# Performance work log

Hardware: AMD Instinct MI355X
Metric: run time of the kernel (lower is better)

Reference implementation:

```python
import jax, jax.numpy as jnp
import numpy as np

EPS = 1e-5
C_M, C, C_Z = 256, 32, 128
N_SEQ, N_RES = 256, 1024


def setup_inputs() -> dict:
    key = jax.random.key(0)
    k1, k2, k3 = jax.random.split(key, 3)
    msa = jax.random.normal(k1, (N_SEQ, N_RES, C_M), dtype=jnp.float32)
    norm_w = jnp.ones((C_M,), dtype=jnp.float32)
    norm_b = jnp.zeros((C_M,), dtype=jnp.float32)
    w_ab = jax.random.normal(k2, (C, C_M), dtype=jnp.float32) * (1.0 / np.sqrt(C_M))
    b_ab = jnp.zeros((C,), dtype=jnp.float32)
    w_out = jax.random.normal(k3, (C_Z, C * C), dtype=jnp.float32) * (1.0 / C)
    b_out = jnp.zeros((C_Z,), dtype=jnp.float32)
    return {"msa": msa, "norm_w": norm_w, "norm_b": norm_b,
            "w_ab": w_ab, "b_ab": b_ab, "w_out": w_out, "b_out": b_out}


def reference(msa, norm_w, norm_b, w_ab, b_ab, w_out, b_out):
    # msa: (s, r, c_m) -> (r, s, c_m)
    x = jnp.transpose(msa, (1, 0, 2))
    s = x.shape[1]
    # LayerNorm over c_m
    mu = jnp.mean(x, axis=-1, keepdims=True)
    var = jnp.mean(jnp.square(x - mu), axis=-1, keepdims=True)
    xn = (x - mu) * jax.lax.rsqrt(var + EPS) * norm_w + norm_b
    # a == b: same linear applied twice to same input in the original
    a = jnp.einsum('rsm,cm->rsc', xn, w_ab) + b_ab          # (r, s, c)
    # mean over s of outer product == batched A^T A / s  -> (r, c, c)
    o = jnp.einsum('rsx,rsy->rxy', a, a) / s
    o = o.reshape(o.shape[0], C * C)                        # (r, c*c)
    pre_pair = jnp.einsum('rk,zk->rz', o, w_out) + b_out    # (r, c_z)
    r = pre_pair.shape[0]
    # unsqueeze(1).expand(r, r, c_z)
    pair = jnp.broadcast_to(pre_pair[:, None, :], (r, r, C_Z))
    return pair
```

## Files before the change

kernel.cpp:

```cpp
#include <hip/hip_runtime.h>

#define NSEQ 256
#define NRES 1024
#define CM   256
#define CC   32
#define CZ   128
#define EPS  1e-5f
#define SROW (NRES * CM)

typedef float f4v __attribute__((ext_vector_type(4)));
typedef __attribute__((ext_vector_type(8))) short short8;
typedef __attribute__((ext_vector_type(4))) float f32x4;
typedef unsigned int u32;

__device__ __forceinline__ float trunc_bf16(float f) {
    return __uint_as_float(__float_as_uint(f) & 0xffff0000u);
}
__device__ __forceinline__ u32 pk_bf16(float a, float b) {
    return (__float_as_uint(b) & 0xffff0000u) | (__float_as_uint(a) >> 16);
}

__global__ void opm_setup(const float* __restrict__ nw,
                          const float* __restrict__ nb,
                          const float* __restrict__ w_ab,
                          const float* __restrict__ b_ab,
                          float* __restrict__ k12,
                          unsigned short* __restrict__ wb_su)
{
    __shared__ float wls[CM * CC];
    const int t = threadIdx.x;
    const float nwm = nw[t];
    #pragma unroll
    for (int c = 0; c < CC; ++c)
        wls[t * CC + c] = nwm * w_ab[c * CM + t];
    __syncthreads();
    if (t < CC) {
        float k1 = 0.f, k2 = 0.f;
        for (int m = 0; m < CM; ++m) {
            k1 += wls[m * CC + t];
            k2 = fmaf(nb[m], w_ab[t * CM + m], k2);
        }
        k12[t]      = k1;
        k12[CC + t] = k2 + b_ab[t];
    }
    for (int e = t; e < 16384; e += 256) {
        const int j     = e & 7;
        const int l     = (e >> 3) & 63;
        const int split = (e >> 9) & 1;
        const int nt    = (e >> 10) & 1;
        const int kk    = e >> 11;
        const int m = (kk << 5) + ((l >> 4) << 3) + j;
        const int c = (nt << 4) + (l & 15);
        const float w  = wls[m * CC + c];
        const float w1 = trunc_bf16(w);
        const float v  = split ? (w - w1) : w;
        wb_su[e] = (unsigned short)(__float_as_uint(v) >> 16);
    }
}

__launch_bounds__(256, 3)
__global__ void opm_compute(const float* __restrict__ msa,
                            const u32*  __restrict__ wb_g,
                            const float* __restrict__ k12,
                            const float* __restrict__ w_out,
                            const float* __restrict__ b_out,
                            float* __restrict__ pre_out)
{
    __shared__ u32 wbl[8192];
    __shared__ float scr[4352];
    __shared__ float st[512];

    const int tid = threadIdx.x;
    const int r   = ((blockIdx.x & 7) << 7) | (blockIdx.x >> 3);
    const int w   = tid >> 6;
    const int l   = tid & 63;
    const int lr  = l & 15;
    const int lk  = l >> 4;

    const float* xr = msa + (size_t)r * CM;
    size_t rowoff[4];
    #pragma unroll
    for (int mt = 0; mt < 4; ++mt)
        rowoff[mt] = (size_t)((w << 6) + (mt << 4) + lr) * SROW + (lk << 3);

    #pragma unroll
    for (int k = 0; k < 8; ++k) {
        const int i = (tid + (k << 8)) << 2;
        *(f4v*)&wbl[i] = *(const f4v*)&wb_g[i];
    }

    f32x4 acc[4][2];
    #pragma unroll
    for (int mt = 0; mt < 4; ++mt) { acc[mt][0] = (f32x4)0.f; acc[mt][1] = (f32x4)0.f; }
    float psum[4], pssq[4];
    #pragma unroll
    for (int mt = 0; mt < 4; ++mt) { psum[mt] = 0.f; pssq[mt] = 0.f; }

    float4 curA[4], curB[4], nxtA[4], nxtB[4];
    #pragma unroll
    for (int mt = 0; mt < 4; ++mt) {
        curA[mt] = *(const float4*)(xr + rowoff[mt]);
        curB[mt] = *(const float4*)(xr + rowoff[mt] + 4);
    }

    __syncthreads();

    #pragma unroll 1
    for (int kk = 0; kk < 8; ++kk) {
        if (kk < 7) {
            const int o = (kk + 1) << 5;
            #pragma unroll
            for (int mt = 0; mt < 4; ++mt) {
                nxtA[mt] = *(const float4*)(xr + rowoff[mt] + o);
                nxtB[mt] = *(const float4*)(xr + rowoff[mt] + o + 4);
            }
        }
        short8 B[2][2];
        #pragma unroll
        for (int nt = 0; nt < 2; ++nt)
            #pragma unroll
            for (int sp = 0; sp < 2; ++sp) {
                const int fb = ((((kk << 1) + nt) << 1) + sp) * 256 + (l << 2);
                B[nt][sp] = __builtin_bit_cast(short8, *(const f4v*)&wbl[fb]);
            }
        #pragma unroll
        for (int mt = 0; mt < 4; ++mt) {
            const float4 pa = curA[mt], pb = curB[mt];
            psum[mt] += ((pa.x + pa.y) + (pa.z + pa.w)) + ((pb.x + pb.y) + (pb.z + pb.w));
            pssq[mt]  = fmaf(pa.x, pa.x, fmaf(pa.y, pa.y, fmaf(pa.z, pa.z, fmaf(pa.w, pa.w, pssq[mt]))));
            pssq[mt]  = fmaf(pb.x, pb.x, fmaf(pb.y, pb.y, fmaf(pb.z, pb.z, fmaf(pb.w, pb.w, pssq[mt]))));
            uint4 u1, u2;
            u1.x = pk_bf16(pa.x, pa.y); u1.y = pk_bf16(pa.z, pa.w);
            u1.z = pk_bf16(pb.x, pb.y); u1.w = pk_bf16(pb.z, pb.w);
            u2.x = pk_bf16(pa.x - trunc_bf16(pa.x), pa.y - trunc_bf16(pa.y));
            u2.y = pk_bf16(pa.z - trunc_bf16(pa.z), pa.w - trunc_bf16(pa.w));
            u2.z = pk_bf16(pb.x - trunc_bf16(pb.x), pb.y - trunc_bf16(pb.y));
            u2.w = pk_bf16(pb.z - trunc_bf16(pb.z), pb.w - trunc_bf16(pb.w));
            const short8 A1 = __builtin_bit_cast(short8, u1);
            const short8 A2 = __builtin_bit_cast(short8, u2);
            acc[mt][0] = __builtin_amdgcn_mfma_f32_16x16x32_bf16(A1, B[0][0], acc[mt][0], 0, 0, 0);
            acc[mt][1] = __builtin_amdgcn_mfma_f32_16x16x32_bf16(A1, B[1][0], acc[mt][1], 0, 0, 0);
            acc[mt][0] = __builtin_amdgcn_mfma_f32_16x16x32_bf16(A1, B[0][1], acc[mt][0], 0, 0, 0);
            acc[mt][1] = __builtin_amdgcn_mfma_f32_16x16x32_bf16(A1, B[1][1], acc[mt][1], 0, 0, 0);
            acc[mt][0] = __builtin_amdgcn_mfma_f32_16x16x32_bf16(A2, B[0][0], acc[mt][0], 0, 0, 0);
            acc[mt][1] = __builtin_amdgcn_mfma_f32_16x16x32_bf16(A2, B[1][0], acc[mt][1], 0, 0, 0);
        }
        if (kk < 7) {
            #pragma unroll
            for (int mt = 0; mt < 4; ++mt) { curA[mt] = nxtA[mt]; curB[mt] = nxtB[mt]; }
        }
    }

    #pragma unroll
    for (int mt = 0; mt < 4; ++mt) {
        float s1 = psum[mt], s2 = pssq[mt];
        s1 += __shfl_xor(s1, 16); s1 += __shfl_xor(s1, 32);
        s2 += __shfl_xor(s2, 16); s2 += __shfl_xor(s2, 32);
        if (l < 16) {
            const int s = (w << 6) + (mt << 4) + lr;
            const float mu  = s1 * (1.f / CM);
            const float var = s2 * (1.f / CM) - mu * mu;
            st[s]       = mu;
            st[256 + s] = 1.f / sqrtf(var + EPS);
        }
    }
    __syncthreads();

    float* aB = (float*)wbl;
    {
        const int cl = lr;
        const float k1_0 = k12[cl],      k1_1 = k12[16 + cl];
        const float k2_0 = k12[CC + cl], k2_1 = k12[CC + 16 + cl];
        #pragma unroll
        for (int mt = 0; mt < 4; ++mt) {
            #pragma unroll
            for (int rg = 0; rg < 4; ++rg) {
                const int s = (w << 6) + (mt << 4) + (lk << 2) + rg;
                const float mu = st[s], rs = st[256 + s];
                const float a0 = fmaf(rs, acc[mt][0][rg] - mu * k1_0, k2_0);
                const float a1 = fmaf(rs, acc[mt][1][rg] - mu * k1_1, k2_1);
                const int sw = s & 7;
                aB[s * CC + (((cl >> 2) ^ sw) << 2) + (cl & 3)]       = a0;
                aB[s * CC + ((((cl >> 2) + 4) ^ sw) << 2) + (cl & 3)] = a1;
            }
        }
    }
    __syncthreads();

    const int grp = w;
    const int xs_ = (tid >> 3) & 7;
    const int ys_ = tid & 7;
    float4 pr0 = {0,0,0,0}, pr1 = {0,0,0,0}, pr2 = {0,0,0,0}, pr3 = {0,0,0,0};
    #pragma unroll 4
    for (int si = 0; si < 64; ++si) {
        const int s  = (grp << 6) + si;
        const int sw = s & 7;
        const float4 ax = *(const float4*)&aB[s * CC + ((xs_ ^ sw) << 2)];
        const float4 ay = *(const float4*)&aB[s * CC + ((ys_ ^ sw) << 2)];
        pr0.x = fmaf(ax.x, ay.x, pr0.x); pr0.y = fmaf(ax.x, ay.y, pr0.y);
        pr0.z = fmaf(ax.x, ay.z, pr0.z); pr0.w = fmaf(ax.x, ay.w, pr0.w);
        pr1.x = fmaf(ax.y, ay.x, pr1.x); pr1.y = fmaf(ax.y, ay.y, pr1.y);
        pr1.z = fmaf(ax.y, ay.z, pr1.z); pr1.w = fmaf(ax.y, ay.w, pr1.w);
        pr2.x = fmaf(ax.z, ay.x, pr2.x); pr2.y = fmaf(ax.z, ay.y, pr2.y);
        pr2.z = fmaf(ax.z, ay.z, pr2.z); pr2.w = fmaf(ax.z, ay.w, pr2.w);
        pr3.x = fmaf(ax.w, ay.x, pr3.x); pr3.y = fmaf(ax.w, ay.y, pr3.y);
        pr3.z = fmaf(ax.w, ay.z, pr3.z); pr3.w = fmaf(ax.w, ay.w, pr3.w);
    }
    {
        float* pb = &scr[(grp << 10) + ((xs_ << 2) * CC) + (ys_ << 2)];
        *(float4*)&pb[0 * CC] = pr0;
        *(float4*)&pb[1 * CC] = pr1;
        *(float4*)&pb[2 * CC] = pr2;
        *(float4*)&pb[3 * CC] = pr3;
    }
    __syncthreads();
    {
        const float inv_s = 1.f / NSEQ;
        float4 a4 = *(const float4*)&scr[(tid << 2)];
        const float4 b1 = *(const float4*)&scr[1024 + (tid << 2)];
        const float4 b2 = *(const float4*)&scr[2048 + (tid << 2)];
        const float4 b3 = *(const float4*)&scr[3072 + (tid << 2)];
        a4.x = (a4.x + b1.x + b2.x + b3.x) * inv_s;
        a4.y = (a4.y + b1.y + b2.y + b3.y) * inv_s;
        a4.z = (a4.z + b1.z + b2.z + b3.z) * inv_s;
        a4.w = (a4.w + b1.w + b2.w + b3.w) * inv_s;
        *(float4*)&scr[tid << 2] = a4;
    }
    __syncthreads();

    {
        const int z    = tid & 127;
        const int half = tid >> 7;
        const float* wrow = w_out + (size_t)z * (CC * CC) + half * 512;
        const float* op   = &scr[half * 512];
        float po = 0.f;
        #pragma unroll 8
        for (int k = 0; k < 512; k += 4) {
            const float4 o4 = *(const float4*)&op[k];
            const float4 w4 = *(const float4*)&wrow[k];
            po = fmaf(o4.x, w4.x, fmaf(o4.y, w4.y, fmaf(o4.z, w4.z, fmaf(o4.w, w4.w, po))));
        }
        scr[4096 + (half << 7) + z] = po;
    }
    __syncthreads();
    if (tid < CZ)
        pre_out[(size_t)r * CZ + tid] = scr[4096 + tid] + scr[4096 + CZ + tid] + b_out[tid];
}

__launch_bounds__(256, 8)
__global__ void opm_bcast(const float* __restrict__ pre,
                          float* __restrict__ out)
{
    const int bid = blockIdx.x;
    const int r   = bid >> 3;
    const int jb  = bid & 7;
    const int z4  = threadIdx.x & 31;
    const int jo  = threadIdx.x >> 5;

    const f4v pv = *((const f4v*)(pre + (size_t)r * CZ) + z4);
    f4v* outp = (f4v*)out + ((size_t)r * NRES + (size_t)jb * 128) * (CZ / 4);
    for (int j0 = 0; j0 < 128; j0 += 8)
        __builtin_nontemporal_store(pv, &outp[(size_t)(j0 + jo) * (CZ / 4) + z4]);
}

extern "C" void kernel_launch(void* const* d_in, const int* in_sizes, int n_in,
                              void* d_out, int out_size, void* d_ws, size_t ws_size,
                              hipStream_t stream) {
    const float* msa   = (const float*)d_in[0];
    const float* nw    = (const float*)d_in[1];
    const float* nb    = (const float*)d_in[2];
    const float* w_ab  = (const float*)d_in[3];
    const float* b_ab  = (const float*)d_in[4];
    const float* w_out = (const float*)d_in[5];
    const float* b_out = (const float*)d_in[6];
    float* out = (float*)d_out;

    float* pre = (float*)d_ws;
    float* k12 = pre + (size_t)NRES * CZ;
    unsigned short* wb_su = (unsigned short*)(k12 + 64);

    opm_setup<<<1, 256, 0, stream>>>(nw, nb, w_ab, b_ab, k12, wb_su);
    opm_compute<<<NRES, 256, 0, stream>>>(msa, (const u32*)wb_su, k12, w_out, b_out, pre);
    opm_bcast<<<NRES * 8, 256, 0, stream>>>(pre, out);
}
```

Measured before the change: 784.2 us.

## Stream MSA chunks into LDS via async global_load_lds double buffering

Replaces the register prefetch of MSA rows with direct global-to-LDS async loads (global_load_lds, 16 bytes per lane) into a double-buffered, XOR-swizzled shared tile, then reads the A fragments from LDS. The weight fragments are now read straight from global or L2 each chunk instead of being staged in LDS, freeing shared memory for the two buffers. The goal is to cut register pressure and hide load latency with async copies. In exchange it adds a barrier per chunk and drops occupancy from 3 to 2 blocks per CU.

```diff
diff --git a/kernel.cpp b/kernel.cpp
--- a/kernel.cpp
+++ b/kernel.cpp
@@ -7,6 +7,7 @@
 #define CZ   128
 #define EPS  1e-5f
 #define SROW (NRES * CM)
+#define CHW  8192
 
 typedef float f4v __attribute__((ext_vector_type(4)));
 typedef __attribute__((ext_vector_type(8))) short short8;
@@ -18,6 +19,12 @@
 }
 __device__ __forceinline__ u32 pk_bf16(float a, float b) {
     return (__float_as_uint(b) & 0xffff0000u) | (__float_as_uint(a) >> 16);
+}
+__device__ __forceinline__ void gload_lds16(const float* g, float* l) {
+    __builtin_amdgcn_global_load_lds(
+        (const __attribute__((address_space(1))) u32*)g,
+        (__attribute__((address_space(3))) u32*)l,
+        16, 0, 0);
 }
 
 __global__ void opm_setup(const float* __restrict__ nw,
@@ -58,7 +65,7 @@
     }
 }
 
-__launch_bounds__(256, 3)
+__launch_bounds__(256, 2)
 __global__ void opm_compute(const float* __restrict__ msa,
                             const u32*  __restrict__ wb_g,
                             const float* __restrict__ k12,
@@ -66,8 +73,7 @@
                             const float* __restrict__ b_out,
                             float* __restrict__ pre_out)
 {
-    __shared__ u32 wbl[8192];
-    __shared__ float scr[4352];
+    __shared__ float xb[2 * CHW];
     __shared__ float st[512];
 
     const int tid = threadIdx.x;
@@ -78,16 +84,10 @@
     const int lk  = l >> 4;
 
     const float* xr = msa + (size_t)r * CM;
-    size_t rowoff[4];
-    #pragma unroll
-    for (int mt = 0; mt < 4; ++mt)
-        rowoff[mt] = (size_t)((w << 6) + (mt << 4) + lr) * SROW + (lk << 3);
-
-    #pragma unroll
-    for (int k = 0; k < 8; ++k) {
-        const int i = (tid + (k << 8)) << 2;
-        *(f4v*)&wbl[i] = *(const f4v*)&wb_g[i];
-    }
+
+    const int srow = (w << 6) + (l >> 3);
+    const int sseg = (l & 7) ^ (l >> 3);
+    const float* gs0 = xr + (size_t)srow * SROW + (sseg << 2);
 
     f32x4 acc[4][2];
     #pragma unroll
@@ -96,36 +96,38 @@
     #pragma unroll
     for (int mt = 0; mt < 4; ++mt) { psum[mt] = 0.f; pssq[mt] = 0.f; }
 
-    float4 curA[4], curB[4], nxtA[4], nxtB[4];
-    #pragma unroll
-    for (int mt = 0; mt < 4; ++mt) {
-        curA[mt] = *(const float4*)(xr + rowoff[mt]);
-        curB[mt] = *(const float4*)(xr + rowoff[mt] + 4);
-    }
-
+    #pragma unroll
+    for (int i = 0; i < 8; ++i)
+        gload_lds16(gs0 + (size_t)(i << 3) * SROW,
+                    &xb[((w << 6) + (i << 3)) << 5]);
     __syncthreads();
 
     #pragma unroll 1
-    for (int kk = 0; kk < 8; ++kk) {
-        if (kk < 7) {
-            const int o = (kk + 1) << 5;
+    for (int c = 0; c < 8; ++c) {
+        float* bR = &xb[(c & 1) ? CHW : 0];
+        if (c < 7) {
+            float* bW = &xb[(c & 1) ? 0 : CHW];
+            const int mb = (c + 1) << 5;
             #pragma unroll
-            for (int mt = 0; mt < 4; ++mt) {
-                nxtA[mt] = *(const float4*)(xr + rowoff[mt] + o);
-                nxtB[mt] = *(const float4*)(xr + rowoff[mt] + o + 4);
-            }
+            for (int i = 0; i < 8; ++i)
+                gload_lds16(gs0 + (size_t)(i << 3) * SROW + mb,
+                            &bW[((w << 6) + (i << 3)) << 5]);
         }
         short8 B[2][2];
         #pragma unroll
         for (int nt = 0; nt < 2; ++nt)
             #pragma unroll
             for (int sp = 0; sp < 2; ++sp) {
-                const int fb = ((((kk << 1) + nt) << 1) + sp) * 256 + (l << 2);
-                B[nt][sp] = __builtin_bit_cast(short8, *(const f4v*)&wbl[fb]);
+                const int fb = ((((c << 1) + nt) << 1) + sp) * 256 + (l << 2);
+                B[nt][sp] = __builtin_bit_cast(short8, *(const f4v*)&wb_g[fb]);
             }
         #pragma unroll
         for (int mt = 0; mt < 4; ++mt) {
-            const float4 pa = curA[mt], pb = curB[mt];
+            const int R  = (w << 6) + (mt << 4) + lr;
+            const int s0 = ((lk << 1)    ) ^ (R & 7);
+            const int s1 = ((lk << 1) | 1) ^ (R & 7);
+            const float4 pa = *(const float4*)&bR[(R << 5) + (s0 << 2)];
+            const float4 pb = *(const float4*)&bR[(R << 5) + (s1 << 2)];
             psum[mt] += ((pa.x + pa.y) + (pa.z + pa.w)) + ((pb.x + pb.y) + (pb.z + pb.w));
             pssq[mt]  = fmaf(pa.x, pa.x, fmaf(pa.y, pa.y, fmaf(pa.z, pa.z, fmaf(pa.w, pa.w, pssq[mt]))));
             pssq[mt]  = fmaf(pb.x, pb.x, fmaf(pb.y, pb.y, fmaf(pb.z, pb.z, fmaf(pb.w, pb.w, pssq[mt]))));
@@ -145,10 +147,7 @@
             acc[mt][0] = __builtin_amdgcn_mfma_f32_16x16x32_bf16(A2, B[0][0], acc[mt][0], 0, 0, 0);
             acc[mt][1] = __builtin_amdgcn_mfma_f32_16x16x32_bf16(A2, B[1][0], acc[mt][1], 0, 0, 0);
         }
-        if (kk < 7) {
-            #pragma unroll
-            for (int mt = 0; mt < 4; ++mt) { curA[mt] = nxtA[mt]; curB[mt] = nxtB[mt]; }
-        }
+        __syncthreads();
     }
 
     #pragma unroll
@@ -166,7 +165,7 @@
     }
     __syncthreads();
 
-    float* aB = (float*)wbl;
+    float* aB = xb;
     {
         const int cl = lr;
         const float k1_0 = k12[cl],      k1_1 = k12[16 + cl];
@@ -187,6 +186,7 @@
     }
     __syncthreads();
 
+    float* scr = xb + CHW;
     const int grp = w;
     const int xs_ = (tid >> 3) & 7;
     const int ys_ = tid & 7;
```

Measured after the change: 795.8 us. Within noise of the previous version (+1.5%).
